# Performance work log

Hardware: AMD Instinct MI355X
Metric: run time of the kernel (lower is better)

## Reference

```python
import jax, jax.numpy as jnp
import numpy as np

DIM_HEAD = 128
HEADS = 16
SCALE = DIM_HEAD ** -0.5


def rotate_half(t):
    # '... (j d) -> ... j d' with j=2: split into first/second halves
    x1, x2 = jnp.split(t, 2, axis=-1)
    return jnp.concatenate((-x2, x1), axis=-1)


def apply_rope(pos, t):
    # pos: [n, d]; t: [..., n, d]
    return t * jnp.cos(pos) + rotate_half(t) * jnp.sin(pos)


def setup_inputs() -> dict:
    key = jax.random.key(0)
    k0, k1, k2, k3 = jax.random.split(key, 4)
    b, n, dim = 2, 2048, 2048
    inner = HEADS * DIM_HEAD
    return {
        "x": jax.random.normal(k0, (b, n, dim), jnp.float32),
        "Wq": jax.random.normal(k1, (dim, inner), jnp.float32) * 0.02,
        "Wkv": jax.random.normal(k2, (dim, 2 * DIM_HEAD), jnp.float32) * 0.02,
        "Wout": jax.random.normal(k3, (inner, dim), jnp.float32) * 0.02,
    }


def reference(x, Wq, Wkv, Wout):
    b, n, dim = x.shape
    # projections from the UN-normalized x (norm in original is dead code)
    q = x @ Wq                               # [b, n, h*d]
    kv = x @ Wkv                             # [b, n, 2d]
    k, v = jnp.split(kv, 2, axis=-1)         # each [b, n, d] (multi-query)
    q = q.reshape(b, n, HEADS, DIM_HEAD).transpose(0, 2, 1, 3)  # [b,h,n,d]

    # rotary positions
    inv_freq = 1.0 / (10000.0 ** (jnp.arange(0, DIM_HEAD, 2, dtype=jnp.float32) / DIM_HEAD))
    freqs = jnp.arange(n, dtype=jnp.float32)[:, None] * inv_freq[None, :]
    pos = jnp.concatenate((freqs, freqs), axis=-1)  # [n, d]

    q = apply_rope(pos, q) * SCALE
    k = apply_rope(pos, k)

    sim = jnp.einsum('bhid,bjd->bhij', q, k)  # [b,h,n,n]
    causal_mask = jnp.triu(jnp.ones((n, n), dtype=bool), 1)
    neg = -jnp.finfo(sim.dtype).max
    sim = jnp.where(causal_mask, neg, sim)
    sim = sim - jax.lax.stop_gradient(jnp.max(sim, axis=-1, keepdims=True))
    attn = jax.nn.softmax(sim, axis=-1)

    out = jnp.einsum('bhij,bjd->bhid', attn, v)          # [b,h,n,d]
    out = out.transpose(0, 2, 1, 3).reshape(b, n, HEADS * DIM_HEAD)
    return out @ Wout
```

## Files before the change

kernel.cpp:

```cpp
#include <hip/hip_runtime.h>
#include <hip/hip_bf16.h>
#include <cstddef>
#include <cstdint>

#define BATCH 2
#define SEQ   2048
#define DIM   2048
#define HEADS 16
#define DHEAD 128
#define INNER (HEADS * DHEAD)
#define MROWS (BATCH * SEQ)
#define ATT_SCALE 0.08838834764831845f
#define QK_SCALE (0.08838834764831845f * 1.4426950408889634f)
#define NEG_LOG2_10000_DIV64 (-13.287712379549449f / 64.0f)
#define M_HAT 12.0f

typedef __attribute__((ext_vector_type(8))) short short8;
typedef __attribute__((ext_vector_type(4))) short short4v;
typedef __attribute__((ext_vector_type(4))) float f32x4;

static __device__ __forceinline__ short f2bf(float x) {
    uint32_t u = __float_as_uint(x);
    uint32_t r = (u + 0x7fffu + ((u >> 16) & 1u)) >> 16;
    return (short)r;
}
static __device__ __forceinline__ float bf2f(short s) {
    return __uint_as_float(((uint32_t)(uint16_t)s) << 16);
}
static __device__ __forceinline__ short2 f2bf2(float a, float b) {
    __hip_bfloat162 h = __float22bfloat162_rn(make_float2(a, b));
    return *reinterpret_cast<short2*>(&h);
}

static __device__ __forceinline__ void glds16(const short* g, short* l) {
    __builtin_amdgcn_global_load_lds(
        (const __attribute__((address_space(1))) unsigned int*)g,
        (__attribute__((address_space(3))) unsigned int*)l, 16, 0, 0);
}

static __device__ __forceinline__ int swz_row(int r) {
    return (r & 3) | ((r >> 1) & 4);
}

static __device__ __forceinline__ void tcast_body(const float* __restrict__ W,
                                                  short* __restrict__ Wt,
                                                  int R, int C, int bx, int by,
                                                  int tid, float (*tile)[65]) {
    const int c0 = bx * 64, r0 = by * 64;
#pragma unroll
    for (int t = 0; t < 4; ++t) {
        int idx = tid + t * 256;
        int row = idx >> 4, col4 = idx & 15;
        float4 v = *(const float4*)&W[(size_t)(r0 + row) * C + c0 + col4 * 4];
        tile[row][col4 * 4 + 0] = v.x;
        tile[row][col4 * 4 + 1] = v.y;
        tile[row][col4 * 4 + 2] = v.z;
        tile[row][col4 * 4 + 3] = v.w;
    }
    __syncthreads();
#pragma unroll
    for (int t = 0; t < 4; ++t) {
        int idx = tid + t * 256;
        int r = idx >> 4, c4 = idx & 15;
        short2 s01 = f2bf2(tile[c4 * 4 + 0][r], tile[c4 * 4 + 1][r]);
        short2 s23 = f2bf2(tile[c4 * 4 + 2][r], tile[c4 * 4 + 3][r]);
        short4v s = {s01.x, s01.y, s23.x, s23.y};
        *(short4v*)&Wt[(size_t)(c0 + r) * R + r0 + c4 * 4] = s;
    }
}

__global__ __launch_bounds__(256) void prep(const float* __restrict__ x,
                                            short* __restrict__ xb,
                                            const float* __restrict__ Wq,
                                            short* __restrict__ Wt,
                                            const float* __restrict__ Wkv,
                                            short* __restrict__ Wkvt,
                                            const float* __restrict__ Wout,
                                            short* __restrict__ WtO,
                                            float2* __restrict__ lut) {
    __shared__ float tile[64][65];
    const int bid = blockIdx.x;
    const int tid = threadIdx.x;
    if (bid < 8192) {
        int i = bid * 256 + tid;
        float4 v = ((const float4*)x)[i];
        short2 s01 = f2bf2(v.x, v.y), s23 = f2bf2(v.z, v.w);
        short4v s = {s01.x, s01.y, s23.x, s23.y};
        ((short4v*)xb)[i] = s;
    } else if (bid < 9216) {
        int t = bid - 8192;
        tcast_body(Wq, Wt, DIM, INNER, t & 31, t >> 5, tid, tile);
    } else if (bid < 9344) {
        int t = bid - 9216;
        tcast_body(Wkv, Wkvt, DIM, 256, t & 3, t >> 2, tid, tile);
    } else if (bid < 10368) {
        int t = bid - 9344;
        tcast_body(Wout, WtO, INNER, DIM, t & 31, t >> 5, tid, tile);
    } else {
        int t = (bid - 10368) * 256 + tid;
        int pos = t >> 6, j = t & 63;
        float ang = (float)pos * exp2f((float)j * NEG_LOG2_10000_DIV64);
        lut[t] = make_float2(cosf(ang), sinf(ang));
    }
}

__global__ __launch_bounds__(256) void gemm_qkv(const short* __restrict__ A,
                                                const short* __restrict__ Bt,
                                                short* __restrict__ qout,
                                                short* __restrict__ kbout,
                                                short* __restrict__ vtout,
                                                const float2* __restrict__ lut) {
    __shared__ __align__(16) short sA[128 * 32];
    __shared__ __align__(16) short sB[128 * 32];
    const int K = DIM;

    const int tid = threadIdx.x;
    const int w = tid >> 6, lane = tid & 63;
    const int ln = lane & 15, qr = lane >> 4;
    const int flat = blockIdx.y * gridDim.x + blockIdx.x;
    const int wg = (flat & 7) * 72 + (flat >> 3);
    const int bm = (wg / 18) * 128, bn = (wg % 18) * 128;
    const int wm = (w >> 1) * 64;
    const int wn2 = (w & 1) * 32;

    const f32x4 zero4 = {0.f, 0.f, 0.f, 0.f};
    f32x4 acc[4][4];
#pragma unroll
    for (int mt = 0; mt < 4; ++mt)
#pragma unroll
        for (int nt = 0; nt < 4; ++nt) acc[mt][nt] = zero4;

    const int srow = lane >> 2;
    const short* pA = A + (size_t)(bm + w * 32 + srow) * K + (lane & 3) * 8;
    const short* pB = Bt + (size_t)(bn + w * 32 + srow) * K + (lane & 3) * 8;
    short* lA = &sA[(w * 32) * 32];
    short* lB = &sB[(w * 32) * 32];

    for (int k0 = 0; k0 < K; k0 += 32) {
        __syncthreads();
        glds16(pA + k0, lA);
        glds16(pA + k0 + (size_t)16 * K, lA + 512);
        glds16(pB + k0, lB);
        glds16(pB + k0 + (size_t)16 * K, lB + 512);
        __syncthreads();

        short8 af[4], bfr[4];
#pragma unroll
        for (int mt = 0; mt < 4; ++mt)
            af[mt] = *(const short8*)&sA[(wm + mt * 16 + ln) * 32 + qr * 8];
#pragma unroll
        for (int nt = 0; nt < 4; ++nt) {
            const int colr = wn2 + ((nt & 1) << 4) + ((nt >> 1) << 6) + ln;
            bfr[nt] = *(const short8*)&sB[colr * 32 + qr * 8];
        }
#pragma unroll
        for (int mt = 0; mt < 4; ++mt)
#pragma unroll
            for (int nt = 0; nt < 4; ++nt)
                acc[mt][nt] = __builtin_amdgcn_mfma_f32_16x16x32_bf16(
                    af[mt], bfr[nt], acc[mt][nt], 0, 0, 0);
    }

    if (bn <= INNER) {
        const float scale = (bn < INNER) ? QK_SCALE : 1.0f;
#pragma unroll
        for (int mt = 0; mt < 4; ++mt) {
#pragma unroll
            for (int nt = 0; nt < 2; ++nt) {
                const int d0 = wn2 + nt * 16 + ln;
#pragma unroll
                for (int r = 0; r < 4; ++r) {
                    const int row = wm + mt * 16 + qr * 4 + r;
                    const int pos = (bm + row) & (SEQ - 1);
                    const float2 cs = lut[pos * 64 + d0];
                    const float a = acc[mt][nt][r];
                    const float b = acc[mt][nt + 2][r];
                    const float lo = (a * cs.x - b * cs.y) * scale;
                    const float hi = (b * cs.x + a * cs.y) * scale;
                    if (bn < INNER) {
                        short* q0 = qout + (size_t)(bm + row) * INNER + bn + d0;
                        q0[0] = f2bf(lo);
                        q0[64] = f2bf(hi);
                    } else {
                        short* k0p = kbout + (size_t)(bm + row) * DHEAD + d0;
                        k0p[0] = f2bf(lo);
                        k0p[64] = f2bf(hi);
                    }
                }
            }
        }
    } else {
        const int gb = bm >> 11;
        const int pos_base = bm & (SEQ - 1);
#pragma unroll
        for (int mt = 0; mt < 4; ++mt) {
#pragma unroll
            for (int nt = 0; nt < 4; ++nt) {
                const int cn = wn2 + ((nt & 1) << 4) + ((nt >> 1) << 6) + ln;
                const int pos0 = pos_base + wm + mt * 16 + qr * 4;
                short2 s01 = f2bf2(acc[mt][nt][0], acc[mt][nt][1]);
                short2 s23 = f2bf2(acc[mt][nt][2], acc[mt][nt][3]);
                short4v sv = {s01.x, s01.y, s23.x, s23.y};
                *(short4v*)&vtout[((size_t)gb * DHEAD + cn) * SEQ + pos0] = sv;
            }
        }
    }
}

__global__ __launch_bounds__(256) void gemm_bt(const short* __restrict__ A,
                                               const short* __restrict__ Bt,
                                               float* __restrict__ C,
                                               int M, int N, int K) {
    __shared__ __align__(16) short sA[128 * 32];
    __shared__ __align__(16) short sB[128 * 32];

    const int tid = threadIdx.x;
    const int w = tid >> 6, lane = tid & 63;
    const int ln = lane & 15, qr = lane >> 4;
    const int flat = blockIdx.y * gridDim.x + blockIdx.x;
    const int wg = (flat & 7) * 64 + (flat >> 3);
    const int bm = (wg >> 4) * 128, bn = (wg & 15) * 128;
    const int wm = (w >> 1) * 64, wn = (w & 1) * 64;

    const f32x4 zero4 = {0.f, 0.f, 0.f, 0.f};
    f32x4 acc[4][4];
#pragma unroll
    for (int mt = 0; mt < 4; ++mt)
#pragma unroll
        for (int nt = 0; nt < 4; ++nt) acc[mt][nt] = zero4;

    const int srow = lane >> 2;
    const short* pA = A + (size_t)(bm + w * 32 + srow) * K + (lane & 3) * 8;
    const short* pB = Bt + (size_t)(bn + w * 32 + srow) * K + (lane & 3) * 8;
    short* lA = &sA[(w * 32) * 32];
    short* lB = &sB[(w * 32) * 32];

    for (int k0 = 0; k0 < K; k0 += 32) {
        __syncthreads();
        glds16(pA + k0, lA);
        glds16(pA + k0 + (size_t)16 * K, lA + 512);
        glds16(pB + k0, lB);
        glds16(pB + k0 + (size_t)16 * K, lB + 512);
        __syncthreads();

        short8 af[4], bfr[4];
#pragma unroll
        for (int mt = 0; mt < 4; ++mt)
            af[mt] = *(const short8*)&sA[(wm + mt * 16 + ln) * 32 + qr * 8];
#pragma unroll
        for (int nt = 0; nt < 4; ++nt)
            bfr[nt] = *(const short8*)&sB[(wn + nt * 16 + ln) * 32 + qr * 8];
#pragma unroll
        for (int mt = 0; mt < 4; ++mt)
#pragma unroll
            for (int nt = 0; nt < 4; ++nt)
                acc[mt][nt] = __builtin_amdgcn_mfma_f32_16x16x32_bf16(
                    af[mt], bfr[nt], acc[mt][nt], 0, 0, 0);
    }

#pragma unroll
    for (int mt = 0; mt < 4; ++mt)
#pragma unroll
        for (int nt = 0; nt < 4; ++nt)
#pragma unroll
            for (int r = 0; r < 4; ++r)
                C[(size_t)(bm + wm + mt * 16 + qr * 4 + r) * N +
                  bn + wn + nt * 16 + ln] = acc[mt][nt][r];
}

__global__ __launch_bounds__(512) void attn_mfma(const short* __restrict__ qb,
                                                 const short* __restrict__ kb,
                                                 const short* __restrict__ vt,
                                                 short* __restrict__ o) {
    __shared__ __align__(16) short sK[2][2][64 * 128];
    __shared__ __align__(16) short sV[2][2][128 * 64];
    __shared__ float lred[4][2][64];

    const int bid = blockIdx.x;
    const int p = bid & 7;
    const int bh = bid >> 3;
    const int h = bh & (HEADS - 1);
    const int b = bh >> 4;

    const int tid = threadIdx.x;
    const int w = tid >> 6;
    const int g = w >> 2;
    const int wg = w & 3;
    const int lane = tid & 63;
    const int ln = lane & 15;
    const int qr = lane >> 4;

    const short* kbase = kb + (size_t)b * SEQ * DHEAD;
    const short* vbase = vt + (size_t)b * DHEAD * SEQ;

    int offK[4], offV[4], ldsK[4], ldsV[4];
#pragma unroll
    for (int t = 0; t < 4; ++t) {
        int rk = wg * 16 + t * 4 + (lane >> 4);
        int ck = (lane & 15) ^ swz_row(rk);
        offK[t] = rk * DHEAD + ck * 8;
        ldsK[t] = (wg * 16 + t * 4) * 128;
        int rv = wg * 32 + t * 8 + (lane >> 3);
        int cv = (lane & 7) ^ swz_row(rv);
        offV[t] = rv * SEQ + cv * 8;
        ldsV[t] = (wg * 32 + t * 8) * 64;
    }

    for (int ph = 0; ph < 2; ++ph) {
        const int it = ph ? p : (15 - p);
        const int i0 = it * 128;
        const int njt = 2 * it + 2;
        const int half = njt >> 1;
        const int igmax = i0 + wg * 32 + 31;

        short8 qf[2][4];
#pragma unroll
        for (int qs = 0; qs < 2; ++qs) {
            const size_t qrow =
                ((size_t)(b * SEQ + i0 + wg * 32 + qs * 16 + ln)) * INNER + h * DHEAD;
#pragma unroll
            for (int ks = 0; ks < 4; ++ks)
                qf[qs][ks] = *(const short8*)&qb[qrow + ks * 32 + qr * 8];
        }

        const f32x4 zero4 = {0.f, 0.f, 0.f, 0.f};
        const f32x4 mhat4 = {-M_HAT, -M_HAT, -M_HAT, -M_HAT};
        f32x4 oa[2][8];
#pragma unroll
        for (int qs = 0; qs < 2; ++qs)
#pragma unroll
            for (int dt = 0; dt < 8; ++dt) oa[qs][dt] = zero4;
        float lsum[2] = {0.f, 0.f};

        __syncthreads();
        {
            const size_t kof = (size_t)g * 64 * DHEAD;
            const size_t vof = (size_t)g * 64;
#pragma unroll
            for (int t = 0; t < 4; ++t)
                glds16(kbase + kof + offK[t], &sK[g][0][ldsK[t]]);
#pragma unroll
            for (int t = 0; t < 4; ++t)
                glds16(vbase + vof + offV[t], &sV[g][0][ldsV[t]]);
        }

        for (int k = 0; k < half; ++k) {
            const int cur = k & 1;
            const int jt = 2 * k + g;
            __syncthreads();
            if (k + 1 < half) {
                const size_t kof = (size_t)(jt + 2) * 64 * DHEAD;
                const size_t vof = (size_t)(jt + 2) * 64;
#pragma unroll
                for (int t = 0; t < 4; ++t)
                    glds16(kbase + kof + offK[t], &sK[g][cur ^ 1][ldsK[t]]);
#pragma unroll
                for (int t = 0; t < 4; ++t)
                    glds16(vbase + vof + offV[t], &sV[g][cur ^ 1][ldsV[t]]);
            }
            if (jt * 64 > igmax) continue;

            f32x4 sacc[2][4];
#pragma unroll
            for (int qs = 0; qs < 2; ++qs)
#pragma unroll
                for (int nt = 0; nt < 4; ++nt) sacc[qs][nt] = mhat4;
            __builtin_amdgcn_s_setprio(1);
#pragma unroll
            for (int nt = 0; nt < 4; ++nt) {
                const int row = ((nt >> 1) << 5) + ((ln >> 2) << 3) +
                                ((nt & 1) << 2) + (ln & 3);
                const int sw = ln & 7;
#pragma unroll
                for (int ks = 0; ks < 4; ++ks) {
                    short8 kf = *(const short8*)&sK[g][cur][row * 128 + ((4 * ks + qr) ^ sw) * 8];
                    sacc[0][nt] = __builtin_amdgcn_mfma_f32_16x16x32_bf16(
                        kf, qf[0][ks], sacc[0][nt], 0, 0, 0);
                    sacc[1][nt] = __builtin_amdgcn_mfma_f32_16x16x32_bf16(
                        kf, qf[1][ks], sacc[1][nt], 0, 0, 0);
                }
            }
            __builtin_amdgcn_s_setprio(0);

            short8 pb[2][2];
#pragma unroll
            for (int qs = 0; qs < 2; ++qs) {
                const int ig = i0 + wg * 32 + qs * 16 + ln;
                if (jt * 64 + 63 > ig) {
#pragma unroll
                    for (int nt = 0; nt < 4; ++nt)
#pragma unroll
                        for (int r = 0; r < 4; ++r) {
                            int jg = jt * 64 + ((nt >> 1) << 5) + qr * 8 +
                                     ((nt & 1) << 2) + r;
                            if (jg > ig) sacc[qs][nt][r] = -3.0e38f;
                        }
                }
                float rs = 0.f;
                float pv[4][4];
#pragma unroll
                for (int nt = 0; nt < 4; ++nt)
#pragma unroll
                    for (int r = 0; r < 4; ++r) {
                        float e = exp2f(sacc[qs][nt][r]);
                        pv[nt][r] = e;
                        rs += e;
                    }
                rs += __shfl_xor(rs, 16);
                rs += __shfl_xor(rs, 32);
                lsum[qs] += rs;
#pragma unroll
                for (int kb2 = 0; kb2 < 2; ++kb2) {
                    short2* pp = (short2*)&pb[qs][kb2];
                    pp[0] = f2bf2(pv[2 * kb2][0], pv[2 * kb2][1]);
                    pp[1] = f2bf2(pv[2 * kb2][2], pv[2 * kb2][3]);
                    pp[2] = f2bf2(pv[2 * kb2 + 1][0], pv[2 * kb2 + 1][1]);
                    pp[3] = f2bf2(pv[2 * kb2 + 1][2], pv[2 * kb2 + 1][3]);
                }
            }

            __builtin_amdgcn_s_setprio(1);
#pragma unroll
            for (int kb2 = 0; kb2 < 2; ++kb2) {
#pragma unroll
                for (int dt = 0; dt < 8; ++dt) {
                    const int row = dt * 16 + ln;
                    short8 vf = *(const short8*)&sV[g][cur][row * 64 +
                        ((4 * kb2 + qr) ^ swz_row(row)) * 8];
                    oa[0][dt] = __builtin_amdgcn_mfma_f32_16x16x32_bf16(
                        vf, pb[0][kb2], oa[0][dt], 0, 0, 0);
                    oa[1][dt] = __builtin_amdgcn_mfma_f32_16x16x32_bf16(
                        vf, pb[1][kb2], oa[1][dt], 0, 0, 0);
                }
            }
            __builtin_amdgcn_s_setprio(0);
        }

        f32x4* cb = (f32x4*)&sK[1][0][0];
        __syncthreads();
        if (g == 1) {
#pragma unroll
            for (int dt = 0; dt < 8; ++dt)
                cb[dt * 256 + wg * 64 + lane] = oa[0][dt];
            lred[wg][0][lane] = lsum[0];
            lred[wg][1][lane] = lsum[1];
        }
        __syncthreads();
        if (g == 0) {
#pragma unroll
            for (int dt = 0; dt < 8; ++dt)
                oa[0][dt] += cb[dt * 256 + wg * 64 + lane];
            lsum[0] += lred[wg][0][lane];
            lsum[1] += lred[wg][1][lane];
        }
        __syncthreads();
        if (g == 1) {
#pragma unroll
            for (int dt = 0; dt < 8; ++dt)
                cb[dt * 256 + wg * 64 + lane] = oa[1][dt];
        }
        __syncthreads();
        if (g == 0) {
#pragma unroll
            for (int dt = 0; dt < 8; ++dt)
                oa[1][dt] += cb[dt * 256 + wg * 64 + lane];
#pragma unroll
            for (int qs = 0; qs < 2; ++qs) {
                const float invl = 1.f / lsum[qs];
                short* orow = o + ((size_t)(b * SEQ + i0 + wg * 32 + qs * 16 + ln)) * INNER +
                              h * DHEAD;
#pragma unroll
                for (int dt = 0; dt < 8; ++dt) {
                    short2 s01 = f2bf2(oa[qs][dt][0] * invl, oa[qs][dt][1] * invl);
                    short2 s23 = f2bf2(oa[qs][dt][2] * invl, oa[qs][dt][3] * invl);
                    short4v sv = {s01.x, s01.y, s23.x, s23.y};
                    *(short4v*)&orow[dt * 16 + qr * 4] = sv;
                }
            }
        }
    }
}

extern "C" void kernel_launch(void* const* d_in, const int* in_sizes, int n_in,
                              void* d_out, int out_size, void* d_ws, size_t ws_size,
                              hipStream_t stream) {
    const float* x    = (const float*)d_in[0];
    const float* Wq   = (const float*)d_in[1];
    const float* Wkv  = (const float*)d_in[2];
    const float* Wout = (const float*)d_in[3];
    float* out = (float*)d_out;

    short* xb    = (short*)d_ws;
    short* Wt    = xb + (size_t)MROWS * DIM;
    short* Wkvt  = Wt + (size_t)DIM * INNER;
    short* WtO   = Wkvt + (size_t)256 * DIM;
    short* qb    = WtO + (size_t)DIM * INNER;
    short* kb    = qb + (size_t)MROWS * INNER;
    short* vt    = kb + (size_t)MROWS * DHEAD;
    float2* lut  = (float2*)(vt + (size_t)BATCH * DHEAD * SEQ);
    short* ob    = xb;

    prep<<<10880, 256, 0, stream>>>(x, xb, Wq, Wt, Wkv, Wkvt, Wout, WtO, lut);
    gemm_qkv<<<dim3(18, 32), 256, 0, stream>>>(xb, Wt, qb, kb, vt, lut);
    attn_mfma<<<256, 512, 0, stream>>>(qb, kb, vt, ob);
    gemm_bt<<<dim3(16, 32), 256, 0, stream>>>(ob, WtO, out, MROWS, DIM, INNER);
}
```

Before: 306.7 us.

## Double-buffer GEMM K-tiles with XOR-swizzled LDS and transpose the RoPE LUT

Both bf16 GEMM kernels now stage 64-wide K tiles into double-buffered LDS, prefetching the next tile while MFMAs run on the current one. LDS rows use an XOR swizzle to avoid bank conflicts, and s_setprio is raised around the MFMA block. The RoPE cos/sin table is transposed to [j][pos], so the QKV epilogue loads four consecutive positions with two float4 reads. The grouped block-index remapping is dropped in favour of plain blockIdx order, which may hurt L2 reuse, and the doubled LDS use may lower occupancy.

```diff
diff --git a/kernel.cpp b/kernel.cpp
--- a/kernel.cpp
+++ b/kernel.cpp
@@ -98,9 +98,10 @@
         tcast_body(Wout, WtO, INNER, DIM, t & 31, t >> 5, tid, tile);
     } else {
         int t = (bid - 10368) * 256 + tid;
-        int pos = t >> 6, j = t & 63;
+        int j = t >> 11;
+        int pos = t & (SEQ - 1);
         float ang = (float)pos * exp2f((float)j * NEG_LOG2_10000_DIV64);
-        lut[t] = make_float2(cosf(ang), sinf(ang));
+        lut[(size_t)j * SEQ + pos] = make_float2(cosf(ang), sinf(ang));
     }
 }
 
@@ -110,16 +111,14 @@
                                                 short* __restrict__ kbout,
                                                 short* __restrict__ vtout,
                                                 const float2* __restrict__ lut) {
-    __shared__ __align__(16) short sA[128 * 32];
-    __shared__ __align__(16) short sB[128 * 32];
+    __shared__ __align__(16) short sA[2][128 * 64];
+    __shared__ __align__(16) short sB[2][128 * 64];
     const int K = DIM;
 
     const int tid = threadIdx.x;
     const int w = tid >> 6, lane = tid & 63;
     const int ln = lane & 15, qr = lane >> 4;
-    const int flat = blockIdx.y * gridDim.x + blockIdx.x;
-    const int wg = (flat & 7) * 72 + (flat >> 3);
-    const int bm = (wg / 18) * 128, bn = (wg % 18) * 128;
+    const int bm = blockIdx.y * 128, bn = blockIdx.x * 128;
     const int wm = (w >> 1) * 64;
     const int wn2 = (w & 1) * 32;
 
@@ -130,53 +129,85 @@
 #pragma unroll
         for (int nt = 0; nt < 4; ++nt) acc[mt][nt] = zero4;
 
-    const int srow = lane >> 2;
-    const short* pA = A + (size_t)(bm + w * 32 + srow) * K + (lane & 3) * 8;
-    const short* pB = Bt + (size_t)(bn + w * 32 + srow) * K + (lane & 3) * 8;
-    short* lA = &sA[(w * 32) * 32];
-    short* lB = &sB[(w * 32) * 32];
-
-    for (int k0 = 0; k0 < K; k0 += 32) {
-        __syncthreads();
-        glds16(pA + k0, lA);
-        glds16(pA + k0 + (size_t)16 * K, lA + 512);
-        glds16(pB + k0, lB);
-        glds16(pB + k0 + (size_t)16 * K, lB + 512);
-        __syncthreads();
-
-        short8 af[4], bfr[4];
-#pragma unroll
-        for (int mt = 0; mt < 4; ++mt)
-            af[mt] = *(const short8*)&sA[(wm + mt * 16 + ln) * 32 + qr * 8];
-#pragma unroll
-        for (int nt = 0; nt < 4; ++nt) {
-            const int colr = wn2 + ((nt & 1) << 4) + ((nt >> 1) << 6) + ln;
-            bfr[nt] = *(const short8*)&sB[colr * 32 + qr * 8];
-        }
-#pragma unroll
-        for (int mt = 0; mt < 4; ++mt)
-#pragma unroll
-            for (int nt = 0; nt < 4; ++nt)
-                acc[mt][nt] = __builtin_amdgcn_mfma_f32_16x16x32_bf16(
-                    af[mt], bfr[nt], acc[mt][nt], 0, 0, 0);
+    int offG[4], ldsO[4];
+#pragma unroll
+    for (int t = 0; t < 4; ++t) {
+        int row = w * 32 + t * 8 + (lane >> 3);
+        int c = (lane & 7) ^ (row & 7);
+        offG[t] = row * K + c * 8;
+        ldsO[t] = (w * 32 + t * 8) * 64;
+    }
+    const short* pA = A + (size_t)bm * K;
+    const short* pB = Bt + (size_t)bn * K;
+
+#pragma unroll
+    for (int t = 0; t < 4; ++t) glds16(pA + offG[t], &sA[0][ldsO[t]]);
+#pragma unroll
+    for (int t = 0; t < 4; ++t) glds16(pB + offG[t], &sB[0][ldsO[t]]);
+    __syncthreads();
+
+    const int NT = K / 64;
+    for (int kt = 0; kt < NT; ++kt) {
+        const int cur = kt & 1;
+        if (kt + 1 < NT) {
+            const int ko = (kt + 1) * 64;
+#pragma unroll
+            for (int t = 0; t < 4; ++t)
+                glds16(pA + ko + offG[t], &sA[cur ^ 1][ldsO[t]]);
+#pragma unroll
+            for (int t = 0; t < 4; ++t)
+                glds16(pB + ko + offG[t], &sB[cur ^ 1][ldsO[t]]);
+        }
+#pragma unroll
+        for (int ks = 0; ks < 2; ++ks) {
+            short8 af[4], bfr[4];
+#pragma unroll
+            for (int mt = 0; mt < 4; ++mt) {
+                const int row = wm + mt * 16 + ln;
+                af[mt] = *(const short8*)&sA[cur][row * 64 +
+                    (((ks << 2) + qr) ^ (row & 7)) * 8];
+            }
+#pragma unroll
+            for (int nt = 0; nt < 4; ++nt) {
+                const int colr = wn2 + ((nt & 1) << 4) + ((nt >> 1) << 6) + ln;
+                bfr[nt] = *(const short8*)&sB[cur][colr * 64 +
+                    (((ks << 2) + qr) ^ (colr & 7)) * 8];
+            }
+            __builtin_amdgcn_s_setprio(1);
+#pragma unroll
+            for (int mt = 0; mt < 4; ++mt)
+#pragma unroll
+                for (int nt = 0; nt < 4; ++nt)
+                    acc[mt][nt] = __builtin_amdgcn_mfma_f32_16x16x32_bf16(
+                        af[mt], bfr[nt], acc[mt][nt], 0, 0, 0);
+            __builtin_amdgcn_s_setprio(0);
+        }
+        __syncthreads();
     }
 
     if (bn <= INNER) {
         const float scale = (bn < INNER) ? QK_SCALE : 1.0f;
 #pragma unroll
+        for (int mt = 0; mt < 2; ++mt) {  }
+#pragma unroll
         for (int mt = 0; mt < 4; ++mt) {
 #pragma unroll
             for (int nt = 0; nt < 2; ++nt) {
                 const int d0 = wn2 + nt * 16 + ln;
+                const int row0 = wm + mt * 16 + qr * 4;
+                const int pos0 = (bm + row0) & (SEQ - 1);
+                const float4* lp = (const float4*)&lut[(size_t)d0 * SEQ + pos0];
+                const float4 c01 = lp[0];
+                const float4 c23 = lp[1];
+                const float cx[4] = {c01.x, c01.z, c23.x, c23.z};
+                const float cy[4] = {c01.y, c01.w, c23.y, c23.w};
 #pragma unroll
                 for (int r = 0; r < 4; ++r) {
-                    const int row = wm + mt * 16 + qr * 4 + r;
-                    const int pos = (bm + row) & (SEQ - 1);
-                    const float2 cs = lut[pos * 64 + d0];
                     const float a = acc[mt][nt][r];
                     const float b = acc[mt][nt + 2][r];
-                    const float lo = (a * cs.x - b * cs.y) * scale;
-                    const float hi = (b * cs.x + a * cs.y) * scale;
+                    const float lo = (a * cx[r] - b * cy[r]) * scale;
+                    const float hi = (b * cx[r] + a * cy[r]) * scale;
+                    const int row = row0 + r;
                     if (bn < INNER) {
                         short* q0 = qout + (size_t)(bm + row) * INNER + bn + d0;
                         q0[0] = f2bf(lo);
@@ -211,15 +242,13 @@
                                                const short* __restrict__ Bt,
                                                float* __restrict__ C,
                                                int M, int N, int K) {
-    __shared__ __align__(16) short sA[128 * 32];
-    __shared__ __align__(16) short sB[128 * 32];
+    __shared__ __align__(16) short sA[2][128 * 64];
+    __shared__ __align__(16) short sB[2][128 * 64];
 
     const int tid = threadIdx.x;
     const int w = tid >> 6, lane = tid & 63;
     const int ln = lane & 15, qr = lane >> 4;
-    const int flat = blockIdx.y * gridDim.x + blockIdx.x;
-    const int wg = (flat & 7) * 64 + (flat >> 3);
-    const int bm = (wg >> 4) * 128, bn = (wg & 15) * 128;
+    const int bm = blockIdx.y * 128, bn = blockIdx.x * 128;
     const int wm = (w >> 1) * 64, wn = (w & 1) * 64;
 
     const f32x4 zero4 = {0.f, 0.f, 0.f, 0.f};
@@ -229,33 +258,60 @@
 #pragma unroll
         for (int nt = 0; nt < 4; ++nt) acc[mt][nt] = zero4;
 
-    const int srow = lane >> 2;
-    const short* pA = A + (size_t)(bm + w * 32 + srow) * K + (lane & 3) * 8;
-    const short* pB = Bt + (size_t)(bn + w * 32 + srow) * K + (lane & 3) * 8;
-    short* lA = &sA[(w * 32) * 32];
-    short* lB = &sB[(w * 32) * 32];
-
-    for (int k0 = 0; k0 < K; k0 += 32) {
-        __syncthreads();
-        glds16(pA + k0, lA);
-        glds16(pA + k0 + (size_t)16 * K, lA + 512);
-        glds16(pB + k0, lB);
-        glds16(pB + k0 + (size_t)16 * K, lB + 512);
-        __syncthreads();
-
-        short8 af[4], bfr[4];
-#pragma unroll
-        for (int mt = 0; mt < 4; ++mt)
-            af[mt] = *(const short8*)&sA[(wm + mt * 16 + ln) * 32 + qr * 8];
-#pragma unroll
-        for (int nt = 0; nt < 4; ++nt)
-            bfr[nt] = *(const short8*)&sB[(wn + nt * 16 + ln) * 32 + qr * 8];
-#pragma unroll
-        for (int mt = 0; mt < 4; ++mt)
-#pragma unroll
-            for (int nt = 0; nt < 4; ++nt)
-                acc[mt][nt] = __builtin_amdgcn_mfma_f32_16x16x32_bf16(
-                    af[mt], bfr[nt], acc[mt][nt], 0, 0, 0);
+    int offG[4], ldsO[4];
+#pragma unroll
+    for (int t = 0; t < 4; ++t) {
+        int row = w * 32 + t * 8 + (lane >> 3);
+        int c = (lane & 7) ^ (row & 7);
+        offG[t] = row * K + c * 8;
+        ldsO[t] = (w * 32 + t * 8) * 64;
+    }
+    const short* pA = A + (size_t)bm * K;
+    const short* pB = Bt + (size_t)bn * K;
+
+#pragma unroll
+    for (int t = 0; t < 4; ++t) glds16(pA + offG[t], &sA[0][ldsO[t]]);
+#pragma unroll
+    for (int t = 0; t < 4; ++t) glds16(pB + offG[t], &sB[0][ldsO[t]]);
+    __syncthreads();
+
+    const int NT = 2048 / 64;
+    for (int kt = 0; kt < NT; ++kt) {
+        const int cur = kt & 1;
+        if (kt + 1 < NT) {
+            const int ko = (kt + 1) * 64;
+#pragma unroll
+            for (int t = 0; t < 4; ++t)
+                glds16(pA + ko + offG[t], &sA[cur ^ 1][ldsO[t]]);
+#pragma unroll
+            for (int t = 0; t < 4; ++t)
+                glds16(pB + ko + offG[t], &sB[cur ^ 1][ldsO[t]]);
+        }
+#pragma unroll
+        for (int ks = 0; ks < 2; ++ks) {
+            short8 af[4], bfr[4];
+#pragma unroll
+            for (int mt = 0; mt < 4; ++mt) {
+                const int row = wm + mt * 16 + ln;
+                af[mt] = *(const short8*)&sA[cur][row * 64 +
+                    (((ks << 2) + qr) ^ (row & 7)) * 8];
+            }
+#pragma unroll
+            for (int nt = 0; nt < 4; ++nt) {
+                const int colr = wn + nt * 16 + ln;
+                bfr[nt] = *(const short8*)&sB[cur][colr * 64 +
+                    (((ks << 2) + qr) ^ (colr & 7)) * 8];
+            }
+            __builtin_amdgcn_s_setprio(1);
+#pragma unroll
+            for (int mt = 0; mt < 4; ++mt)
+#pragma unroll
+                for (int nt = 0; nt < 4; ++nt)
+                    acc[mt][nt] = __builtin_amdgcn_mfma_f32_16x16x32_bf16(
+                        af[mt], bfr[nt], acc[mt][nt], 0, 0, 0);
+            __builtin_amdgcn_s_setprio(0);
+        }
+        __syncthreads();
     }
 
 #pragma unroll
```

Result: faster. 291.4 us (-5.0%).
